# Performance work log

Measured on AMD Instinct MI355X. Metric: run time of the kernel, lower is better.

Reference implementation:

```python
import jax, jax.numpy as jnp
import numpy as np

B, H, G = 65536, 256, 7  # batch, hidden_dim, number of gates


def setup_inputs() -> dict:
    key = jax.random.key(0)
    k0, k1, k2, k3, k4, k5 = jax.random.split(key, 6)
    inter_times = jax.random.uniform(k0, (B,), dtype=jnp.float32)
    h_ti = jax.random.uniform(k1, (B, H), dtype=jnp.float32)
    c_ti = jax.random.uniform(k2, (B, H), dtype=jnp.float32)
    cbar = jax.random.uniform(k3, (B, H), dtype=jnp.float32)
    # 7 gate Linear layers stacked: order = input, forget, output, ibar, fbar, z, decay
    W = jax.random.normal(k4, (G, H, H), dtype=jnp.float32) * (1.0 / np.sqrt(H))
    b = jax.random.normal(k5, (G, H), dtype=jnp.float32) * 0.02
    return {"inter_times": inter_times, "h_ti": h_ti, "c_ti": c_ti, "cbar": cbar, "W": W, "b": b}


def reference(inter_times, h_ti, c_ti, cbar, W, b):
    # Batched GEMM for all 7 gates at once: torch Linear computes x @ W.T + b
    gates = jnp.einsum('bh,goh->gbo', h_ti, W) + b[:, None, :]  # [7,B,H]
    i_g = jax.nn.sigmoid(gates[0])
    f_g = jax.nn.sigmoid(gates[1])
    o_g = jax.nn.sigmoid(gates[2])
    ibar_g = jax.nn.sigmoid(gates[3])
    fbar_g = jax.nn.sigmoid(gates[4])
    z = jnp.tanh(gates[5])
    decay_t = jax.nn.softplus(gates[6])
    # decayed cell memory c(t) = cbar + (c - cbar) * exp(-decay * dt)
    dt = inter_times[:, None]  # [B,1]
    c_t_after = cbar + (c_ti - cbar) * jnp.exp(-decay_t * dt)
    c_new = f_g * c_t_after + i_g * z
    cbar_new = fbar_g * cbar + ibar_g * z
    h_new = o_g * jnp.tanh(c_t_after)
    return (o_g, h_new, c_new, cbar_new, decay_t)
```

## Files before the change

### kernel.cpp

```cpp
#include <hip/hip_runtime.h>
#include <hip/hip_bf16.h>
#include <cstddef>

#define BATCH 65536
#define HDIM  256
#define NGATE 7
#define BH    ((size_t)BATCH * HDIM)

typedef __bf16 bf16x8 __attribute__((ext_vector_type(8)));
typedef __bf16 bf16x4 __attribute__((ext_vector_type(4)));
typedef float  f32x4  __attribute__((ext_vector_type(4)));

__global__ void __launch_bounds__(256) cvt_w_kernel(const float* __restrict__ W,
                                                    __bf16* __restrict__ Wb) {
    int i = (blockIdx.x * 256 + threadIdx.x) * 4;
    float4 v = *(const float4*)(W + i);
    bf16x4 r;
    r[0] = (__bf16)v.x; r[1] = (__bf16)v.y; r[2] = (__bf16)v.z; r[3] = (__bf16)v.w;
    *(bf16x4*)(Wb + i) = r;
}

__device__ __forceinline__ float sigmoidf_(float x) {
    return __builtin_amdgcn_rcpf(1.0f + __expf(-x));
}
__device__ __forceinline__ float tanhf_(float x) {
    return 1.0f - 2.0f * __builtin_amdgcn_rcpf(1.0f + __expf(2.0f * x));
}
__device__ __forceinline__ float softplusf_(float x) {
    return fmaxf(x, 0.0f) + __logf(1.0f + __expf(-fabsf(x)));
}

__global__ void __launch_bounds__(256)
fused_ctlstm(const float* __restrict__ inter_times,
             const float* __restrict__ h_ti,
             const float* __restrict__ c_ti,
             const float* __restrict__ cbar,
             const __bf16* __restrict__ Wb,
             const float* __restrict__ bias,
             float* __restrict__ out) {
    const int tid  = threadIdx.x;
    const int lane = tid & 63;
    const int wave = tid >> 6;
    const int col  = lane & 15;
    const int quad = lane >> 4;
    const int m0   = blockIdx.x * 64;

#pragma unroll 1
    for (int ot = 0; ot < 4; ++ot) {
        const int o0 = (wave * 4 + ot) * 16;
        const int o  = o0 + col;

        f32x4 acc[NGATE][4];
#pragma unroll
        for (int g = 0; g < NGATE; ++g)
#pragma unroll
            for (int mf = 0; mf < 4; ++mf)
                acc[g][mf] = (f32x4){0.0f, 0.0f, 0.0f, 0.0f};

#pragma unroll
        for (int ks = 0; ks < 8; ++ks) {
            const int k0 = ks * 32 + quad * 8;

            bf16x8 afrag[4];
#pragma unroll
            for (int mf = 0; mf < 4; ++mf) {
                const float* ap = h_ti + (size_t)(m0 + mf * 16 + col) * HDIM + k0;
                float4 lo = *(const float4*)(ap);
                float4 hi = *(const float4*)(ap + 4);
                afrag[mf][0] = (__bf16)lo.x; afrag[mf][1] = (__bf16)lo.y;
                afrag[mf][2] = (__bf16)lo.z; afrag[mf][3] = (__bf16)lo.w;
                afrag[mf][4] = (__bf16)hi.x; afrag[mf][5] = (__bf16)hi.y;
                afrag[mf][6] = (__bf16)hi.z; afrag[mf][7] = (__bf16)hi.w;
            }

#pragma unroll
            for (int g = 0; g < NGATE; ++g) {
                bf16x8 bfrag = *(const bf16x8*)(Wb + ((size_t)g * HDIM + o) * HDIM + k0);
#pragma unroll
                for (int mf = 0; mf < 4; ++mf)
                    acc[g][mf] = __builtin_amdgcn_mfma_f32_16x16x32_bf16(
                        afrag[mf], bfrag, acc[g][mf], 0, 0, 0);
            }
        }

        float bv[NGATE];
#pragma unroll
        for (int g = 0; g < NGATE; ++g) bv[g] = bias[g * HDIM + o];

#pragma unroll
        for (int mf = 0; mf < 4; ++mf) {
#pragma unroll
            for (int r = 0; r < 4; ++r) {
                const int row = m0 + mf * 16 + quad * 4 + r;
                const size_t idx = (size_t)row * HDIM + o;

                const float i_g  = sigmoidf_(acc[0][mf][r] + bv[0]);
                const float f_g  = sigmoidf_(acc[1][mf][r] + bv[1]);
                const float o_g  = sigmoidf_(acc[2][mf][r] + bv[2]);
                const float ib_g = sigmoidf_(acc[3][mf][r] + bv[3]);
                const float fb_g = sigmoidf_(acc[4][mf][r] + bv[4]);
                const float z    = tanhf_(acc[5][mf][r] + bv[5]);
                const float dec  = softplusf_(acc[6][mf][r] + bv[6]);

                const float dt = inter_times[row];
                const float ct = c_ti[idx];
                const float cb = cbar[idx];

                const float c_after  = cb + (ct - cb) * __expf(-dec * dt);
                const float c_new    = f_g * c_after + i_g * z;
                const float cbar_new = fb_g * cb + ib_g * z;
                const float h_new    = o_g * tanhf_(c_after);

                out[idx]            = o_g;
                out[BH + idx]       = h_new;
                out[2 * BH + idx]   = c_new;
                out[3 * BH + idx]   = cbar_new;
                out[4 * BH + idx]   = dec;
            }
        }
    }
}

extern "C" void kernel_launch(void* const* d_in, const int* in_sizes, int n_in,
                              void* d_out, int out_size, void* d_ws, size_t ws_size,
                              hipStream_t stream) {
    const float* inter_times = (const float*)d_in[0];
    const float* h_ti        = (const float*)d_in[1];
    const float* c_ti        = (const float*)d_in[2];
    const float* cbar        = (const float*)d_in[3];
    const float* W           = (const float*)d_in[4];
    const float* bias        = (const float*)d_in[5];
    float* out = (float*)d_out;

    __bf16* Wb = (__bf16*)d_ws;

    cvt_w_kernel<<<(NGATE * HDIM * HDIM) / (256 * 4), 256, 0, stream>>>(W, Wb);

    fused_ctlstm<<<BATCH / 64, 256, 0, stream>>>(inter_times, h_ti, c_ti, cbar,
                                                 Wb, bias, out);
}
```

Before: 779.1 us.

## Swap MFMA operands so each wave owns 16 batch rows and emits vector stores

Each wave now takes 16 batch rows and keeps their h rows in registers as bf16 for the whole kernel, instead of reloading and reconverting h fragments for every output tile. Weights become the A operand, so the accumulator lanes hold 4 consecutive output columns. This allows vectorised float4 loads of c_ti, cbar and bias, and float4 nontemporal stores of all five outputs. Weight fragments are now loaded once per 16 rows rather than amortised over 64, which raises weight traffic from L2. Launch bounds also request 4 blocks per SM.

```diff
diff --git a/kernel.cpp b/kernel.cpp
--- a/kernel.cpp
+++ b/kernel.cpp
@@ -30,7 +30,7 @@
     return fmaxf(x, 0.0f) + __logf(1.0f + __expf(-fabsf(x)));
 }
 
-__global__ void __launch_bounds__(256)
+__global__ void __launch_bounds__(256, 4)
 fused_ctlstm(const float* __restrict__ inter_times,
              const float* __restrict__ h_ti,
              const float* __restrict__ c_ti,
@@ -43,81 +43,81 @@
     const int wave = tid >> 6;
     const int col  = lane & 15;
     const int quad = lane >> 4;
-    const int m0   = blockIdx.x * 64;
+
+    const int b = blockIdx.x * 64 + wave * 16 + col;
+    const float dt = inter_times[b];
+
+    bf16x8 bfrag[8];
+    {
+        const float* hp = h_ti + (size_t)b * HDIM + quad * 8;
+#pragma unroll
+        for (int ks = 0; ks < 8; ++ks) {
+            float4 lo = *(const float4*)(hp + ks * 32);
+            float4 hi = *(const float4*)(hp + ks * 32 + 4);
+            bf16x8 v;
+            v[0] = (__bf16)lo.x; v[1] = (__bf16)lo.y;
+            v[2] = (__bf16)lo.z; v[3] = (__bf16)lo.w;
+            v[4] = (__bf16)hi.x; v[5] = (__bf16)hi.y;
+            v[6] = (__bf16)hi.z; v[7] = (__bf16)hi.w;
+            bfrag[ks] = v;
+        }
+    }
 
 #pragma unroll 1
-    for (int ot = 0; ot < 4; ++ot) {
-        const int o0 = (wave * 4 + ot) * 16;
-        const int o  = o0 + col;
+    for (int ot = 0; ot < 16; ++ot) {
+        const int o0   = ot * 16;
+        const int orow = o0 + quad * 4;
+        const size_t idx = (size_t)b * HDIM + orow;
 
-        f32x4 acc[NGATE][4];
+        const f32x4 ct4 = *(const f32x4*)(c_ti + idx);
+        const f32x4 cb4 = *(const f32x4*)(cbar + idx);
+
+        f32x4 acc[NGATE];
 #pragma unroll
-        for (int g = 0; g < NGATE; ++g)
-#pragma unroll
-            for (int mf = 0; mf < 4; ++mf)
-                acc[g][mf] = (f32x4){0.0f, 0.0f, 0.0f, 0.0f};
+        for (int g = 0; g < NGATE; ++g) acc[g] = (f32x4){0.f, 0.f, 0.f, 0.f};
 
 #pragma unroll
         for (int ks = 0; ks < 8; ++ks) {
-            const int k0 = ks * 32 + quad * 8;
-
-            bf16x8 afrag[4];
-#pragma unroll
-            for (int mf = 0; mf < 4; ++mf) {
-                const float* ap = h_ti + (size_t)(m0 + mf * 16 + col) * HDIM + k0;
-                float4 lo = *(const float4*)(ap);
-                float4 hi = *(const float4*)(ap + 4);
-                afrag[mf][0] = (__bf16)lo.x; afrag[mf][1] = (__bf16)lo.y;
-                afrag[mf][2] = (__bf16)lo.z; afrag[mf][3] = (__bf16)lo.w;
-                afrag[mf][4] = (__bf16)hi.x; afrag[mf][5] = (__bf16)hi.y;
-                afrag[mf][6] = (__bf16)hi.z; afrag[mf][7] = (__bf16)hi.w;
-            }
-
+            const __bf16* wp = Wb + (size_t)(o0 + col) * HDIM + ks * 32 + quad * 8;
 #pragma unroll
             for (int g = 0; g < NGATE; ++g) {
-                bf16x8 bfrag = *(const bf16x8*)(Wb + ((size_t)g * HDIM + o) * HDIM + k0);
-#pragma unroll
-                for (int mf = 0; mf < 4; ++mf)
-                    acc[g][mf] = __builtin_amdgcn_mfma_f32_16x16x32_bf16(
-                        afrag[mf], bfrag, acc[g][mf], 0, 0, 0);
+                bf16x8 afrag = *(const bf16x8*)(wp + (size_t)g * HDIM * HDIM);
+                acc[g] = __builtin_amdgcn_mfma_f32_16x16x32_bf16(
+                    afrag, bfrag[ks], acc[g], 0, 0, 0);
             }
         }
 
-        float bv[NGATE];
 #pragma unroll
-        for (int g = 0; g < NGATE; ++g) bv[g] = bias[g * HDIM + o];
+        for (int g = 0; g < NGATE; ++g)
+            acc[g] += *(const f32x4*)(bias + g * HDIM + orow);
 
+        f32x4 og4, hn4, cn4, cbn4, dec4;
 #pragma unroll
-        for (int mf = 0; mf < 4; ++mf) {
-#pragma unroll
-            for (int r = 0; r < 4; ++r) {
-                const int row = m0 + mf * 16 + quad * 4 + r;
-                const size_t idx = (size_t)row * HDIM + o;
+        for (int r = 0; r < 4; ++r) {
+            const float i_g  = sigmoidf_(acc[0][r]);
+            const float f_g  = sigmoidf_(acc[1][r]);
+            const float o_g  = sigmoidf_(acc[2][r]);
+            const float ib_g = sigmoidf_(acc[3][r]);
+            const float fb_g = sigmoidf_(acc[4][r]);
+            const float z    = tanhf_(acc[5][r]);
+            const float dec  = softplusf_(acc[6][r]);
 
-                const float i_g  = sigmoidf_(acc[0][mf][r] + bv[0]);
-                const float f_g  = sigmoidf_(acc[1][mf][r] + bv[1]);
-                const float o_g  = sigmoidf_(acc[2][mf][r] + bv[2]);
-                const float ib_g = sigmoidf_(acc[3][mf][r] + bv[3]);
-                const float fb_g = sigmoidf_(acc[4][mf][r] + bv[4]);
-                const float z    = tanhf_(acc[5][mf][r] + bv[5]);
-                const float dec  = softplusf_(acc[6][mf][r] + bv[6]);
+            const float ct = ct4[r];
+            const float cb = cb4[r];
 
-                const float dt = inter_times[row];
-                const float ct = c_ti[idx];
-                const float cb = cbar[idx];
+            const float c_after = cb + (ct - cb) * __expf(-dec * dt);
+            og4[r]  = o_g;
+            hn4[r]  = o_g * tanhf_(c_after);
+            cn4[r]  = f_g * c_after + i_g * z;
+            cbn4[r] = fb_g * cb + ib_g * z;
+            dec4[r] = dec;
+        }
 
-                const float c_after  = cb + (ct - cb) * __expf(-dec * dt);
-                const float c_new    = f_g * c_after + i_g * z;
-                const float cbar_new = fb_g * cb + ib_g * z;
-                const float h_new    = o_g * tanhf_(c_after);
-
-                out[idx]            = o_g;
-                out[BH + idx]       = h_new;
-                out[2 * BH + idx]   = c_new;
-                out[3 * BH + idx]   = cbar_new;
-                out[4 * BH + idx]   = dec;
-            }
-        }
+        __builtin_nontemporal_store(og4,  (f32x4*)(out + idx));
+        __builtin_nontemporal_store(hn4,  (f32x4*)(out + BH + idx));
+        __builtin_nontemporal_store(cn4,  (f32x4*)(out + 2 * BH + idx));
+        __builtin_nontemporal_store(cbn4, (f32x4*)(out + 3 * BH + idx));
+        __builtin_nontemporal_store(dec4, (f32x4*)(out + 4 * BH + idx));
     }
 }
 
```

Result: slower. 823.3 us (+5.7%).
